# Kernel optimization log

Hardware: AMD Instinct MI355X
Metric: run time of the kernel (lower is better)

## Reference

```python
import jax, jax.numpy as jnp
import numpy as np

N, C, H, W = 8, 64, 128, 128
K2 = 9  # 3x3 kernel
BN_EPS = 1e-5


def conv3x3(x, w):
    # x: [N,Ci,H,W], w: [Co,Ci,3,3], stride 1, padding 1, dilation 1
    return jax.lax.conv_general_dilated(
        x, w, window_strides=(1, 1), padding=((1, 1), (1, 1)),
        dimension_numbers=('NCHW', 'OIHW', 'NCHW'))


def deform_conv3x3(x, offset, w):
    # torchvision deform_conv2d v1 (no mask), stride 1, pad 1, dil 1, 1 group.
    # offset: [N, 2*K2, H, W] ordered (dy, dx) per kernel tap.
    n, c, h, wd = x.shape
    off = offset.reshape(n, K2, 2, h, wd)
    k = jnp.arange(3) - 1  # kernel tap displacements with pad=1
    ky, kx = jnp.meshgrid(k, k, indexing='ij')
    ky = ky.reshape(K2).astype(x.dtype)
    kx = kx.reshape(K2).astype(x.dtype)
    ys = jnp.arange(h, dtype=x.dtype)
    xs = jnp.arange(wd, dtype=x.dtype)
    # sampling positions: [N, K2, H, W]
    py = ys[None, None, :, None] + ky[None, :, None, None] + off[:, :, 0]
    px = xs[None, None, None, :] + kx[None, :, None, None] + off[:, :, 1]
    y0f = jnp.floor(py)
    x0f = jnp.floor(px)
    wy1 = py - y0f
    wx1 = px - x0f
    y0 = y0f.astype(jnp.int32)
    x0 = x0f.astype(jnp.int32)
    xflat = x.reshape(n, c, h * wd)

    def corner(yc, xc, wgt):
        valid = ((yc >= 0) & (yc < h) & (xc >= 0) & (xc < wd)).astype(x.dtype)
        idx = jnp.clip(yc, 0, h - 1) * wd + jnp.clip(xc, 0, wd - 1)  # [N,K2,H,W]
        gath = jax.vmap(lambda xf, i: jnp.take(xf, i.reshape(-1), axis=1)
                        .reshape(c, K2, h, wd))(xflat, idx)  # [N,C,K2,H,W]
        return gath * (wgt * valid)[:, None]

    samp = (corner(y0, x0, (1 - wy1) * (1 - wx1))
            + corner(y0, x0 + 1, (1 - wy1) * wx1)
            + corner(y0 + 1, x0, wy1 * (1 - wx1))
            + corner(y0 + 1, x0 + 1, wy1 * wx1))  # [N,C,K2,H,W]
    return jnp.einsum('nckhw,ock->nohw', samp, w.reshape(w.shape[0], c, K2))


def setup_inputs() -> dict:
    key = jax.random.key(0)
    ks = jax.random.split(key, 5)
    x = jax.random.normal(ks[0], (N, C, H, W), dtype=jnp.float32)
    # small offset-conv weights so predicted offsets stay within a few pixels
    w_off = jax.random.normal(ks[1], (2 * K2 + 9, C, 3, 3), dtype=jnp.float32) * 0.01
    w_def = jax.random.normal(ks[2], (C, C, 3, 3), dtype=jnp.float32) * (1.0 / np.sqrt(C * 9))
    w1 = jax.random.normal(ks[3], (K2, C, 3, 3), dtype=jnp.float32) * (1.0 / np.sqrt(C * 9))
    gamma = jnp.ones((K2,), jnp.float32)
    beta = jnp.zeros((K2,), jnp.float32)
    mean = jnp.zeros((K2,), jnp.float32)
    var = jnp.ones((K2,), jnp.float32)
    return {"x": x, "w_off": w_off, "w_def": w_def, "w1": w1,
            "gamma": gamma, "beta": beta, "mean": mean, "var": var}


def reference(x, w_off, w_def, w1, gamma, beta, mean, var):
    off_filter = conv3x3(x, w_off)            # [N, 27, H, W]
    offset = off_filter[:, :2 * K2]           # [N, 18, H, W]
    filt = off_filter[:, -K2:]                # [N, 9, H, W]
    out = deform_conv3x3(x, offset, w_def)    # [N, C, H, W]
    xr = x + out
    h = conv3x3(xr, w1)                       # [N, 9, H, W]
    # BatchNorm2d (inference form with running stats)
    h = (h - mean[None, :, None, None]) * jax.lax.rsqrt(var[None, :, None, None] + BN_EPS)
    h = h * gamma[None, :, None, None] + beta[None, :, None, None]
    h = jnp.maximum(h, 0.0)
    return (h, filt)
```

## Files before the change

kernel.cpp:

```cpp
#include <hip/hip_runtime.h>
#include <cmath>

#define H_ 128
#define W_ 128
#define HW_ 16384
#define C_ 64
#define N_ 8
#define BN_EPS 1e-5f

typedef __attribute__((ext_vector_type(8))) short short8;
typedef __attribute__((ext_vector_type(4))) float float4_;

__device__ inline short f2bf(float f) {
    unsigned u = __builtin_bit_cast(unsigned, f);
    u += 0x7fffu + ((u >> 16) & 1u);
    return (short)(u >> 16);
}
__device__ inline float bf2f(short s) {
    unsigned u = ((unsigned)(unsigned short)s) << 16;
    return __builtin_bit_cast(float, u);
}

#define OFFB_OFS   0
#define XB8_OFS    9437184
#define XR8_OFS    26214400
#define WDEFB_OFS  42991616
#define BT27_OFS   43065344
#define BT9_OFS    43102720

__global__ __launch_bounds__(256) void prep_w(
    const float* __restrict__ w_off, const float* __restrict__ w_def,
    const float* __restrict__ w1, short* __restrict__ wdefB,
    short* __restrict__ bt27, short* __restrict__ bt9)
{
    int i = blockIdx.x * 256 + threadIdx.x;
    if (i < 36864) {
        int o = i / 576, r = i - o*576, t = r >> 6, c = r & 63;
        wdefB[i] = f2bf(w_def[o*576 + c*9 + t]);
    } else if (i < 36864 + 18688) {
        int j = i - 36864;
        int oc = j / 584, K = j - oc*584;
        float v = 0.f;
        if (oc < 27 && K < 576) { int t = K >> 6, c = K & 63; v = w_off[oc*576 + c*9 + t]; }
        bt27[j] = f2bf(v);
    } else if (i < 36864 + 18688 + 9344) {
        int j = i - 36864 - 18688;
        int oc = j / 584, K = j - oc*584;
        float v = 0.f;
        if (oc < 9 && K < 576) { int t = K >> 6, c = K & 63; v = w1[oc*576 + c*9 + t]; }
        bt9[j] = f2bf(v);
    }
}

__global__ __launch_bounds__(256) void convert_x(
    const float* __restrict__ x, short8* __restrict__ xb8)
{
    int idx = blockIdx.x * 256 + threadIdx.x;
    int pix = idx & (HW_-1);
    int c8  = (idx >> 14) & 7;
    int n   = idx >> 17;
    const float* xp = x + ((size_t)(n*64 + c8*8))*HW_ + pix;
    short8 v;
    #pragma unroll
    for (int j = 0; j < 8; j++) v[j] = f2bf(xp[j*HW_]);
    xb8[idx] = v;
}

__global__ __launch_bounds__(256) void conv27_mfma(
    const short8* __restrict__ xb8, const short* __restrict__ bt_g,
    float* __restrict__ off_buf, float* __restrict__ filt_out)
{
    __shared__ short8 patch[8*325];
    __shared__ short8 btl[32*73];
    const int tid = threadIdx.x;
    const int bx = blockIdx.x, by = blockIdx.y, n = blockIdx.z;

    for (int i = tid; i < 2336; i += 256) btl[i] = ((const short8*)bt_g)[i];
    for (int i = tid; i < 2592; i += 256) {
        int c8 = i / 324, r = i - c8*324;
        int py = r / 18, px = r - py*18;
        int gy = by*16 - 1 + py, gx = bx*16 - 1 + px;
        short8 v = {0,0,0,0,0,0,0,0};
        if ((unsigned)gy < 128u && (unsigned)gx < 128u)
            v = xb8[(size_t)(n*8 + c8)*HW_ + gy*W_ + gx];
        patch[c8*325 + py*18 + px] = v;
    }
    __syncthreads();

    const int lane = tid & 63, wid = tid >> 6;
    const int q = lane >> 4, col = lane & 15;
    float4_ acc[4][2];
    #pragma unroll
    for (int i = 0; i < 4; i++) {
        acc[i][0] = (float4_){0.f,0.f,0.f,0.f};
        acc[i][1] = (float4_){0.f,0.f,0.f,0.f};
    }

    #pragma unroll 2
    for (int k0 = 0; k0 < 18; k0++) {
        int t = k0 >> 1;
        int dy = t/3, dx = t - dy*3;
        int c8 = (k0 & 1)*4 + q;
        short8 b0 = btl[col*73 + k0*4 + q];
        short8 b1 = btl[(16 + col)*73 + k0*4 + q];
        #pragma unroll
        for (int i = 0; i < 4; i++) {
            int mt = wid*4 + i;
            short8 a = patch[c8*325 + (mt + dy)*18 + (col + dx)];
            acc[i][0] = __builtin_amdgcn_mfma_f32_16x16x32_bf16(a, b0, acc[i][0], 0,0,0);
            acc[i][1] = __builtin_amdgcn_mfma_f32_16x16x32_bf16(a, b1, acc[i][1], 0,0,0);
        }
    }

    #pragma unroll
    for (int i = 0; i < 4; i++) {
        int ty = wid*4 + i;
        #pragma unroll
        for (int nt = 0; nt < 2; nt++) {
            int oc = nt*16 + col;
            if (oc >= 27) continue;
            #pragma unroll
            for (int reg = 0; reg < 4; reg++) {
                int tx = q*4 + reg;
                int pix = (by*16 + ty)*W_ + bx*16 + tx;
                float v = acc[i][nt][reg];
                if (oc < 18) off_buf[((size_t)n*18 + oc)*HW_ + pix] = v;
                else         filt_out[((size_t)n*9 + (oc-18))*HW_ + pix] = v;
            }
        }
    }
}

__global__ __launch_bounds__(256, 2) void deform_mfma(
    const float* __restrict__ off_buf, const short8* __restrict__ xb8,
    const short8* __restrict__ wdefB, short* __restrict__ xr8s)
{
    __shared__ short8 patch[8*484];
    const int tid = threadIdx.x;
    const int bx = blockIdx.x, by = blockIdx.y, n = blockIdx.z;
    const int lane = tid & 63, wid = tid >> 6;
    const int q = lane >> 4, col = lane & 15;
    const int r0 = by*16 - 3, c0 = bx*16 - 3;
    const float*  ob    = off_buf + (size_t)n*18*HW_;
    const short8* xbase = xb8 + (size_t)n*8*HW_;
    const short*  xbs   = (const short*)xbase;

    for (int i = tid; i < 3872; i += 256) {
        int c8 = i / 484, r = i - c8*484;
        int py = r / 22, px = r - py*22;
        int gy = r0 + py, gx = c0 + px;
        short8 v = {0,0,0,0,0,0,0,0};
        if ((unsigned)gy < 128u && (unsigned)gx < 128u)
            v = xbase[(size_t)c8*HW_ + gy*W_ + gx];
        patch[c8*484 + r] = v;
    }
    __syncthreads();

    const int gxc = bx*16 + col;
    int pixi[4];
    #pragma unroll
    for (int i = 0; i < 4; i++) pixi[i] = (by*16 + wid*4 + i)*W_ + gxc;

    float4_ acc[4][4];
    #pragma unroll
    for (int i = 0; i < 4; i++)
        #pragma unroll
        for (int nt = 0; nt < 4; nt++) acc[i][nt] = (float4_){0.f,0.f,0.f,0.f};

    float oy[4], ox[4];
    #pragma unroll
    for (int i = 0; i < 4; i++) { oy[i] = ob[pixi[i]]; ox[i] = ob[HW_ + pixi[i]]; }

    #pragma unroll 1
    for (int t = 0; t < 9; t++) {
        const int dy = t/3 - 1, dx = (t - (t/3)*3) - 1;
        float oyn[4], oxn[4];
        if (t < 8) {
            #pragma unroll
            for (int i = 0; i < 4; i++) {
                oyn[i] = ob[(2*t+2)*HW_ + pixi[i]];
                oxn[i] = ob[(2*t+3)*HW_ + pixi[i]];
            }
        }
        short8 afrag[4][2];
        #pragma unroll
        for (int i = 0; i < 4; i++) {
            const int gy = by*16 + wid*4 + i;
            float py = (float)(gy + dy) + oy[i];
            float px = (float)(gxc + dx) + ox[i];
            float y0f = floorf(py), x0f = floorf(px);
            float wy1 = py - y0f, wx1 = px - x0f;
            float wy0 = 1.f - wy1, wx0 = 1.f - wx1;
            int y0 = (int)y0f, x0 = (int)x0f;
            int y1 = y0 + 1,   x1 = x0 + 1;
            float vy0 = ((unsigned)y0 < (unsigned)H_) ? 1.f : 0.f;
            float vy1 = ((unsigned)y1 < (unsigned)H_) ? 1.f : 0.f;
            float vx0 = ((unsigned)x0 < (unsigned)W_) ? 1.f : 0.f;
            float vx1 = ((unsigned)x1 < (unsigned)W_) ? 1.f : 0.f;
            float w00 = wy0*wx0*vy0*vx0, w01 = wy0*wx1*vy0*vx1;
            float w10 = wy1*wx0*vy1*vx0, w11 = wy1*wx1*vy1*vx1;
            int cy0 = min(max(y0, 0), H_-1), cy1 = min(max(y1, 0), H_-1);
            int cx0 = min(max(x0, 0), W_-1), cx1 = min(max(x1, 0), W_-1);
            int ly0 = cy0 - r0, ly1 = cy1 - r0;
            int lx0 = cx0 - c0, lx1 = cx1 - c0;
            bool inp = ((unsigned)ly0 < 22u) & ((unsigned)ly1 < 22u)
                     & ((unsigned)lx0 < 22u) & ((unsigned)lx1 < 22u);
            #pragma unroll
            for (int ks = 0; ks < 2; ks++) {
                const int c8 = ks*4 + q;
                short8 p00, p01, p10, p11;
                if (inp) {
                    const short8* pl = &patch[c8*484];
                    p00 = pl[ly0*22 + lx0]; p01 = pl[ly0*22 + lx1];
                    p10 = pl[ly1*22 + lx0]; p11 = pl[ly1*22 + lx1];
                } else {
                    const short8* xg = xbase + (size_t)c8*HW_;
                    p00 = xg[cy0*W_ + cx0]; p01 = xg[cy0*W_ + cx1];
                    p10 = xg[cy1*W_ + cx0]; p11 = xg[cy1*W_ + cx1];
                }
                short8 a;
                #pragma unroll
                for (int j = 0; j < 8; j++) {
                    float s = bf2f(p00[j])*w00 + bf2f(p01[j])*w01
                            + bf2f(p10[j])*w10 + bf2f(p11[j])*w11;
                    a[j] = f2bf(s);
                }
                afrag[i][ks] = a;
            }
        }
        #pragma unroll
        for (int ks = 0; ks < 2; ks++) {
            #pragma unroll
            for (int nt = 0; nt < 4; nt++) {
                short8 b = wdefB[(size_t)(nt*16 + col)*72 + t*8 + ks*4 + q];
                #pragma unroll
                for (int i = 0; i < 4; i++)
                    acc[i][nt] = __builtin_amdgcn_mfma_f32_16x16x32_bf16(
                        afrag[i][ks], b, acc[i][nt], 0,0,0);
            }
        }
        #pragma unroll
        for (int i = 0; i < 4; i++) { oy[i] = oyn[i]; ox[i] = oxn[i]; }
    }

    short* xout = xr8s + (size_t)n*8*HW_*8;
    #pragma unroll
    for (int i = 0; i < 4; i++) {
        const int gy = by*16 + wid*4 + i;
        #pragma unroll
        for (int nt = 0; nt < 4; nt++) {
            const int o = nt*16 + col;
            #pragma unroll
            for (int reg = 0; reg < 4; reg++) {
                const int gx = bx*16 + q*4 + reg;
                const int pix = gy*W_ + gx;
                size_t si = ((size_t)(o >> 3)*HW_ + pix)*8 + (o & 7);
                float r = bf2f(xbs[si]);
                xout[si] = f2bf(acc[i][nt][reg] + r);
            }
        }
    }
}

__global__ __launch_bounds__(256) void conv9_mfma(
    const short8* __restrict__ xr8, const short* __restrict__ bt_g,
    const float* __restrict__ gamma, const float* __restrict__ beta,
    const float* __restrict__ mean, const float* __restrict__ var,
    float* __restrict__ out)
{
    __shared__ short8 patch[8*325];
    __shared__ short8 btl[16*73];
    const int tid = threadIdx.x;
    const int bx = blockIdx.x, by = blockIdx.y, n = blockIdx.z;

    for (int i = tid; i < 1168; i += 256) btl[i] = ((const short8*)bt_g)[i];
    for (int i = tid; i < 2592; i += 256) {
        int c8 = i / 324, r = i - c8*324;
        int py = r / 18, px = r - py*18;
        int gy = by*16 - 1 + py, gx = bx*16 - 1 + px;
        short8 v = {0,0,0,0,0,0,0,0};
        if ((unsigned)gy < 128u && (unsigned)gx < 128u)
            v = xr8[(size_t)(n*8 + c8)*HW_ + gy*W_ + gx];
        patch[c8*325 + py*18 + px] = v;
    }
    __syncthreads();

    const int lane = tid & 63, wid = tid >> 6;
    const int q = lane >> 4, col = lane & 15;
    float4_ acc[4];
    #pragma unroll
    for (int i = 0; i < 4; i++) acc[i] = (float4_){0.f,0.f,0.f,0.f};

    #pragma unroll 2
    for (int k0 = 0; k0 < 18; k0++) {
        int t = k0 >> 1;
        int dy = t/3, dx = t - dy*3;
        int c8 = (k0 & 1)*4 + q;
        short8 b0 = btl[col*73 + k0*4 + q];
        #pragma unroll
        for (int i = 0; i < 4; i++) {
            int mt = wid*4 + i;
            short8 a = patch[c8*325 + (mt + dy)*18 + (col + dx)];
            acc[i] = __builtin_amdgcn_mfma_f32_16x16x32_bf16(a, b0, acc[i], 0,0,0);
        }
    }

    float sc = 0.f, sh = 0.f;
    if (col < 9) {
        sc = gamma[col] * rsqrtf(var[col] + BN_EPS);
        sh = beta[col] - mean[col] * sc;
    }
    #pragma unroll
    for (int i = 0; i < 4; i++) {
        int ty = wid*4 + i;
        if (col < 9) {
            #pragma unroll
            for (int reg = 0; reg < 4; reg++) {
                int tx = q*4 + reg;
                int pix = (by*16 + ty)*W_ + bx*16 + tx;
                float h = fmaxf(fmaf(acc[i][reg], sc, sh), 0.f);
                out[((size_t)n*9 + col)*HW_ + pix] = h;
            }
        }
    }
}

extern "C" void kernel_launch(void* const* d_in, const int* in_sizes, int n_in,
                              void* d_out, int out_size, void* d_ws, size_t ws_size,
                              hipStream_t stream)
{
    const float* x     = (const float*)d_in[0];
    const float* w_off = (const float*)d_in[1];
    const float* w_def = (const float*)d_in[2];
    const float* w1    = (const float*)d_in[3];
    const float* gamma = (const float*)d_in[4];
    const float* beta  = (const float*)d_in[5];
    const float* mean  = (const float*)d_in[6];
    const float* var   = (const float*)d_in[7];
    float* out = (float*)d_out;

    char* ws = (char*)d_ws;
    float*  off_buf = (float*)(ws + OFFB_OFS);
    short8* xb8     = (short8*)(ws + XB8_OFS);
    short8* xr8     = (short8*)(ws + XR8_OFS);
    short*  wdefB   = (short*)(ws + WDEFB_OFS);
    short*  bt27    = (short*)(ws + BT27_OFS);
    short*  bt9     = (short*)(ws + BT9_OFS);

    float* h_out    = out;
    float* filt_out = out + (size_t)N_ * 9 * HW_;

    prep_w<<<dim3(254), dim3(256), 0, stream>>>(w_off, w_def, w1, wdefB, bt27, bt9);
    convert_x<<<dim3(4096), dim3(256), 0, stream>>>(x, xb8);

    dim3 cgrid(8, 8, 8);
    conv27_mfma<<<cgrid, dim3(256), 0, stream>>>(xb8, bt27, off_buf, filt_out);
    deform_mfma<<<cgrid, dim3(256), 0, stream>>>(off_buf, xb8, (const short8*)wdefB, (short*)xr8);
    conv9_mfma<<<cgrid, dim3(256), 0, stream>>>(xr8, bt9, gamma, beta, mean, var, h_out);
}
```

Before: 172.0 us.

## Double threads per block, drop LDS weight staging, vectorize output stores

All three conv kernels now launch 512 threads per block, with each wave covering 2 tile rows instead of 4. This halves the per-thread accumulators and work and gives more waves to hide the latency of the deform gather. Weight fragments are read straight from global memory instead of being staged in LDS, which removes that copy and its LDS footprint. The trade is more global or L2 traffic for weights. Output stores in conv27 and conv9 become float4 vector stores.

```diff
diff --git a/kernel.cpp b/kernel.cpp
--- a/kernel.cpp
+++ b/kernel.cpp
@@ -66,17 +66,15 @@
     xb8[idx] = v;
 }
 
-__global__ __launch_bounds__(256) void conv27_mfma(
-    const short8* __restrict__ xb8, const short* __restrict__ bt_g,
+__global__ __launch_bounds__(512, 4) void conv27_mfma(
+    const short8* __restrict__ xb8, const short8* __restrict__ btg,
     float* __restrict__ off_buf, float* __restrict__ filt_out)
 {
     __shared__ short8 patch[8*325];
-    __shared__ short8 btl[32*73];
     const int tid = threadIdx.x;
     const int bx = blockIdx.x, by = blockIdx.y, n = blockIdx.z;
 
-    for (int i = tid; i < 2336; i += 256) btl[i] = ((const short8*)bt_g)[i];
-    for (int i = tid; i < 2592; i += 256) {
+    for (int i = tid; i < 2592; i += 512) {
         int c8 = i / 324, r = i - c8*324;
         int py = r / 18, px = r - py*18;
         int gy = by*16 - 1 + py, gx = bx*16 - 1 + px;
@@ -89,9 +87,9 @@
 
     const int lane = tid & 63, wid = tid >> 6;
     const int q = lane >> 4, col = lane & 15;
-    float4_ acc[4][2];
-    #pragma unroll
-    for (int i = 0; i < 4; i++) {
+    float4_ acc[2][2];
+    #pragma unroll
+    for (int i = 0; i < 2; i++) {
         acc[i][0] = (float4_){0.f,0.f,0.f,0.f};
         acc[i][1] = (float4_){0.f,0.f,0.f,0.f};
     }
@@ -101,11 +99,11 @@
         int t = k0 >> 1;
         int dy = t/3, dx = t - dy*3;
         int c8 = (k0 & 1)*4 + q;
-        short8 b0 = btl[col*73 + k0*4 + q];
-        short8 b1 = btl[(16 + col)*73 + k0*4 + q];
-        #pragma unroll
-        for (int i = 0; i < 4; i++) {
-            int mt = wid*4 + i;
+        short8 b0 = btg[col*73 + k0*4 + q];
+        short8 b1 = btg[(16 + col)*73 + k0*4 + q];
+        #pragma unroll
+        for (int i = 0; i < 2; i++) {
+            int mt = wid*2 + i;
             short8 a = patch[c8*325 + (mt + dy)*18 + (col + dx)];
             acc[i][0] = __builtin_amdgcn_mfma_f32_16x16x32_bf16(a, b0, acc[i][0], 0,0,0);
             acc[i][1] = __builtin_amdgcn_mfma_f32_16x16x32_bf16(a, b1, acc[i][1], 0,0,0);
@@ -113,25 +111,23 @@
     }
 
     #pragma unroll
-    for (int i = 0; i < 4; i++) {
-        int ty = wid*4 + i;
+    for (int i = 0; i < 2; i++) {
+        int gy = by*16 + wid*2 + i;
+        int pix0 = gy*W_ + bx*16 + q*4;
         #pragma unroll
         for (int nt = 0; nt < 2; nt++) {
             int oc = nt*16 + col;
             if (oc >= 27) continue;
-            #pragma unroll
-            for (int reg = 0; reg < 4; reg++) {
-                int tx = q*4 + reg;
-                int pix = (by*16 + ty)*W_ + bx*16 + tx;
-                float v = acc[i][nt][reg];
-                if (oc < 18) off_buf[((size_t)n*18 + oc)*HW_ + pix] = v;
-                else         filt_out[((size_t)n*9 + (oc-18))*HW_ + pix] = v;
-            }
-        }
-    }
-}
-
-__global__ __launch_bounds__(256, 2) void deform_mfma(
+            float4_ v = acc[i][nt];
+            if (oc < 18)
+                *(float4_*)&off_buf[((size_t)n*18 + oc)*HW_ + pix0] = v;
+            else
+                *(float4_*)&filt_out[((size_t)n*9 + (oc-18))*HW_ + pix0] = v;
+        }
+    }
+}
+
+__global__ __launch_bounds__(512, 4) void deform_mfma(
     const float* __restrict__ off_buf, const short8* __restrict__ xb8,
     const short8* __restrict__ wdefB, short* __restrict__ xr8s)
 {
@@ -145,7 +141,7 @@
     const short8* xbase = xb8 + (size_t)n*8*HW_;
     const short*  xbs   = (const short*)xbase;
 
-    for (int i = tid; i < 3872; i += 256) {
+    for (int i = tid; i < 3872; i += 512) {
         int c8 = i / 484, r = i - c8*484;
         int py = r / 22, px = r - py*22;
         int gy = r0 + py, gx = c0 + px;
@@ -157,35 +153,35 @@
     __syncthreads();
 
     const int gxc = bx*16 + col;
-    int pixi[4];
-    #pragma unroll
-    for (int i = 0; i < 4; i++) pixi[i] = (by*16 + wid*4 + i)*W_ + gxc;
-
-    float4_ acc[4][4];
-    #pragma unroll
-    for (int i = 0; i < 4; i++)
+    int pixi[2];
+    #pragma unroll
+    for (int i = 0; i < 2; i++) pixi[i] = (by*16 + wid*2 + i)*W_ + gxc;
+
+    float4_ acc[2][4];
+    #pragma unroll
+    for (int i = 0; i < 2; i++)
         #pragma unroll
         for (int nt = 0; nt < 4; nt++) acc[i][nt] = (float4_){0.f,0.f,0.f,0.f};
 
-    float oy[4], ox[4];
-    #pragma unroll
-    for (int i = 0; i < 4; i++) { oy[i] = ob[pixi[i]]; ox[i] = ob[HW_ + pixi[i]]; }
+    float oy[2], ox[2];
+    #pragma unroll
+    for (int i = 0; i < 2; i++) { oy[i] = ob[pixi[i]]; ox[i] = ob[HW_ + pixi[i]]; }
 
     #pragma unroll 1
     for (int t = 0; t < 9; t++) {
         const int dy = t/3 - 1, dx = (t - (t/3)*3) - 1;
-        float oyn[4], oxn[4];
+        float oyn[2], oxn[2];
         if (t < 8) {
             #pragma unroll
-            for (int i = 0; i < 4; i++) {
+            for (int i = 0; i < 2; i++) {
                 oyn[i] = ob[(2*t+2)*HW_ + pixi[i]];
                 oxn[i] = ob[(2*t+3)*HW_ + pixi[i]];
             }
         }
-        short8 afrag[4][2];
-        #pragma unroll
-        for (int i = 0; i < 4; i++) {
-            const int gy = by*16 + wid*4 + i;
+        short8 afrag[2][2];
+        #pragma unroll
+        for (int i = 0; i < 2; i++) {
+            const int gy = by*16 + wid*2 + i;
             float py = (float)(gy + dy) + oy[i];
             float px = (float)(gxc + dx) + ox[i];
             float y0f = floorf(py), x0f = floorf(px);
@@ -234,19 +230,19 @@
             for (int nt = 0; nt < 4; nt++) {
                 short8 b = wdefB[(size_t)(nt*16 + col)*72 + t*8 + ks*4 + q];
                 #pragma unroll
-                for (int i = 0; i < 4; i++)
+                for (int i = 0; i < 2; i++)
                     acc[i][nt] = __builtin_amdgcn_mfma_f32_16x16x32_bf16(
                         afrag[i][ks], b, acc[i][nt], 0,0,0);
             }
         }
         #pragma unroll
-        for (int i = 0; i < 4; i++) { oy[i] = oyn[i]; ox[i] = oxn[i]; }
+        for (int i = 0; i < 2; i++) { oy[i] = oyn[i]; ox[i] = oxn[i]; }
     }
 
     short* xout = xr8s + (size_t)n*8*HW_*8;
     #pragma unroll
-    for (int i = 0; i < 4; i++) {
-        const int gy = by*16 + wid*4 + i;
+    for (int i = 0; i < 2; i++) {
+        const int gy = by*16 + wid*2 + i;
         #pragma unroll
         for (int nt = 0; nt < 4; nt++) {
             const int o = nt*16 + col;
@@ -262,19 +258,17 @@
     }
 }
 
-__global__ __launch_bounds__(256) void conv9_mfma(
-    const short8* __restrict__ xr8, const short* __restrict__ bt_g,
+__global__ __launch_bounds__(512, 4) void conv9_mfma(
+    const short8* __restrict__ xr8, const short8* __restrict__ btg,
     const float* __restrict__ gamma, const float* __restrict__ beta,
     const float* __restrict__ mean, const float* __restrict__ var,
     float* __restrict__ out)
 {
     __shared__ short8 patch[8*325];
-    __shared__ short8 btl[16*73];
     const int tid = threadIdx.x;
     const int bx = blockIdx.x, by = blockIdx.y, n = blockIdx.z;
 
-    for (int i = tid; i < 1168; i += 256) btl[i] = ((const short8*)bt_g)[i];
-    for (int i = tid; i < 2592; i += 256) {
+    for (int i = tid; i < 2592; i += 512) {
         int c8 = i / 324, r = i - c8*324;
         int py = r / 18, px = r - py*18;
         int gy = by*16 - 1 + py, gx = bx*16 - 1 + px;
@@ -287,19 +281,19 @@
 
     const int lane = tid & 63, wid = tid >> 6;
     const int q = lane >> 4, col = lane & 15;
-    float4_ acc[4];
-    #pragma unroll
-    for (int i = 0; i < 4; i++) acc[i] = (float4_){0.f,0.f,0.f,0.f};
+    float4_ acc[2];
+    #pragma unroll
+    for (int i = 0; i < 2; i++) acc[i] = (float4_){0.f,0.f,0.f,0.f};
 
     #pragma unroll 2
     for (int k0 = 0; k0 < 18; k0++) {
         int t = k0 >> 1;
         int dy = t/3, dx = t - dy*3;
         int c8 = (k0 & 1)*4 + q;
-        short8 b0 = btl[col*73 + k0*4 + q];
-        #pragma unroll
-        for (int i = 0; i < 4; i++) {
-            int mt = wid*4 + i;
+        short8 b0 = btg[col*73 + k0*4 + q];
+        #pragma unroll
+        for (int i = 0; i < 2; i++) {
+            int mt = wid*2 + i;
             short8 a = patch[c8*325 + (mt + dy)*18 + (col + dx)];
             acc[i] = __builtin_amdgcn_mfma_f32_16x16x32_bf16(a, b0, acc[i], 0,0,0);
         }
@@ -311,16 +305,15 @@
         sh = beta[col] - mean[col] * sc;
     }
     #pragma unroll
-    for (int i = 0; i < 4; i++) {
-        int ty = wid*4 + i;
+    for (int i = 0; i < 2; i++) {
+        int gy = by*16 + wid*2 + i;
         if (col < 9) {
-            #pragma unroll
-            for (int reg = 0; reg < 4; reg++) {
-                int tx = q*4 + reg;
-                int pix = (by*16 + ty)*W_ + bx*16 + tx;
-                float h = fmaxf(fmaf(acc[i][reg], sc, sh), 0.f);
-                out[((size_t)n*9 + col)*HW_ + pix] = h;
-            }
+            int pix0 = gy*W_ + bx*16 + q*4;
+            float4_ v;
+            #pragma unroll
+            for (int reg = 0; reg < 4; reg++)
+                v[reg] = fmaxf(fmaf(acc[i][reg], sc, sh), 0.f);
+            *(float4_*)&out[((size_t)n*9 + col)*HW_ + pix0] = v;
         }
     }
 }
@@ -354,7 +347,7 @@
     convert_x<<<dim3(4096), dim3(256), 0, stream>>>(x, xb8);
 
     dim3 cgrid(8, 8, 8);
-    conv27_mfma<<<cgrid, dim3(256), 0, stream>>>(xb8, bt27, off_buf, filt_out);
-    deform_mfma<<<cgrid, dim3(256), 0, stream>>>(off_buf, xb8, (const short8*)wdefB, (short*)xr8);
-    conv9_mfma<<<cgrid, dim3(256), 0, stream>>>(xr8, bt9, gamma, beta, mean, var, h_out);
-}
+    conv27_mfma<<<cgrid, dim3(512), 0, stream>>>(xb8, (const short8*)bt27, off_buf, filt_out);
+    deform_mfma<<<cgrid, dim3(512), 0, stream>>>(off_buf, xb8, (const short8*)wdefB, (short*)xr8);
+    conv9_mfma<<<cgrid, dim3(512), 0, stream>>>(xr8, (const short8*)bt9, gamma, beta, mean, var, h_out);
+}
```

Measured after the change: 185.6 us. 7.9% more time.
